# Kernel tuning notes

Measured on AMD Instinct MI355X. Metric: run time of the kernel, lower is better.

## Reference

```python
import jax, jax.numpy as jnp
import numpy as np

B, C, P = 16, 512, 4096


def setup_inputs() -> dict:
    key = jax.random.key(0)
    ks = jax.random.split(key, 7)
    s = 1.0 / np.sqrt(C)  # torch Conv1d default init scale
    return {
        "x": jax.random.normal(ks[0], (B, C, P), dtype=jnp.float32),
        "Wq": jax.random.uniform(ks[1], (C, C), jnp.float32, -s, s),
        "bq": jax.random.uniform(ks[2], (C,), jnp.float32, -s, s),
        "Wk": jax.random.uniform(ks[3], (C, C), jnp.float32, -s, s),
        "bk": jax.random.uniform(ks[4], (C,), jnp.float32, -s, s),
        "Wv": jax.random.uniform(ks[5], (C, C), jnp.float32, -s, s),
        "bv": jax.random.uniform(ks[6], (C,), jnp.float32, -s, s),
    }


def reference(x, Wq, bq, Wk, bk, Wv, bv):
    # 1x1 Conv1d == channel-mixing GEMM: out[b,o,p] = sum_i W[o,i] x[b,i,p] + b[o]
    q = jnp.einsum('oi,bip->bop', Wq, x) + bq[None, :, None]   # [B,C,P]
    k = jnp.einsum('oi,bip->bop', Wk, x) + bk[None, :, None]   # [B,C,P]
    v = jnp.einsum('oi,bip->bop', Wv, x) + bv[None, :, None]   # [B,C,P]
    energy = jnp.einsum('bcp,bdp->bcd', q, k)                  # [B,C,C] (unscaled)
    attn = jax.nn.softmax(energy, axis=-1)
    out = jnp.einsum('bcd,bdp->bcp', attn, v)                  # [B,C,P]
    return out
```

## Files before the change

kernel.cpp:

```cpp
#include <hip/hip_runtime.h>
#include <hip/hip_bf16.h>

#define CD 512
#define PD 4096
#define BD 16
#define GKS 8
#define NTRI 10

typedef __bf16 bf16x8 __attribute__((ext_vector_type(8)));
typedef float f32x4 __attribute__((ext_vector_type(4)));
typedef unsigned short u16x8 __attribute__((ext_vector_type(8)));
typedef unsigned short u16x4 __attribute__((ext_vector_type(4)));

__device__ __forceinline__ unsigned short f2bf(float f) {
  unsigned u = __builtin_bit_cast(unsigned, f);
  u += 0x7FFFu + ((u >> 16) & 1u);
  return (unsigned short)(u >> 16);
}
__device__ __forceinline__ float bf2f(unsigned short h) {
  unsigned u = ((unsigned)h) << 16;
  return __builtin_bit_cast(float, u);
}

__global__ void convert_w2(const float* __restrict__ Wq, const float* __restrict__ Wk,
                           const float* __restrict__ Wv,
                           unsigned short* __restrict__ Wqh, unsigned short* __restrict__ Wql,
                           unsigned short* __restrict__ Wkh, unsigned short* __restrict__ Wkl,
                           unsigned short* __restrict__ Wvh) {
  int i = blockIdx.x * 256 + threadIdx.x;
  if (i >= CD * CD) return;
  float q = Wq[i]; unsigned short qh = f2bf(q);
  Wqh[i] = qh; Wql[i] = f2bf(q - bf2f(qh));
  float k = Wk[i]; unsigned short kh = f2bf(k);
  Wkh[i] = kh; Wkl[i] = f2bf(k - bf2f(kh));
  Wvh[i] = f2bf(Wv[i]);
}

__global__ void convert_x(const float* __restrict__ x, unsigned short* __restrict__ xsh,
                          unsigned short* __restrict__ xsl, unsigned short* __restrict__ xth,
                          float* __restrict__ r_part) {
  __shared__ float tile[64][65];
  int z = blockIdx.z;
  int c0 = blockIdx.y * 64, p0 = blockIdx.x * 64;
  const float* xb = x + (size_t)z * CD * PD;
  int t = threadIdx.x;
  int tr = t >> 4, tc = t & 15;
  float psum[4];
#pragma unroll
  for (int j = 0; j < 4; ++j) {
    int r = tr + j * 16;
    const float* src = xb + (size_t)(c0 + r) * PD + p0 + tc * 4;
    float s = 0.f;
#pragma unroll
    for (int i = 0; i < 4; ++i) {
      float v = src[i];
      tile[r][tc * 4 + i] = v;
      s += v;
    }
    psum[j] = s;
  }
#pragma unroll
  for (int j = 0; j < 4; ++j) {
    float s = psum[j];
    s += __shfl_xor(s, 1);
    s += __shfl_xor(s, 2);
    s += __shfl_xor(s, 4);
    s += __shfl_xor(s, 8);
    if (tc == 0)
      r_part[((size_t)z * CD + c0 + tr + j * 16) * 64 + (p0 >> 6)] = s;
  }
  __syncthreads();
#pragma unroll
  for (int j = 0; j < 4; ++j) {
    int r = tr + j * 16;
    u16x4 hv, lv;
#pragma unroll
    for (int i = 0; i < 4; ++i) {
      float v = tile[r][tc * 4 + i];
      unsigned short h = f2bf(v);
      hv[i] = h; lv[i] = f2bf(v - bf2f(h));
    }
    size_t o = (size_t)z * CD * PD + (size_t)(c0 + r) * PD + p0 + tc * 4;
    *reinterpret_cast<u16x4*>(xsh + o) = hv;
    *reinterpret_cast<u16x4*>(xsl + o) = lv;
  }
#pragma unroll
  for (int j = 0; j < 4; ++j) {
    int pr = tr + j * 16;
    u16x4 hv;
#pragma unroll
    for (int i = 0; i < 4; ++i) hv[i] = f2bf(tile[tc * 4 + i][pr]);
    size_t o = (size_t)z * PD * CD + (size_t)(p0 + pr) * CD + c0 + tc * 4;
    *reinterpret_cast<u16x4*>(xth + o) = hv;
  }
}

__global__ void uvw_kernel(const float* __restrict__ r_part, const float* __restrict__ Wq,
                           const float* __restrict__ bq, const float* __restrict__ Wk,
                           float* __restrict__ uw) {
  __shared__ float rl[CD];
  int z = blockIdx.x, rg = blockIdx.y;
  int t = threadIdx.x;
  for (int c = t; c < CD; c += 256) {
    const float* rp = r_part + ((size_t)z * CD + c) * 64;
    f32x4 s4 = *reinterpret_cast<const f32x4*>(rp);
#pragma unroll
    for (int pb = 4; pb < 64; pb += 4) s4 += *reinterpret_cast<const f32x4*>(rp + pb);
    rl[c] = s4[0] + s4[1] + s4[2] + s4[3];
  }
  __syncthreads();
  int lane = t & 63, w = t >> 6;
#pragma unroll
  for (int rr = 0; rr < 16; ++rr) {
    int c = rg * 64 + w * 16 + rr;
    const float* wq = Wq + (size_t)c * CD;
    const float* wk = Wk + (size_t)c * CD;
    float du = 0.f, dw = 0.f;
#pragma unroll
    for (int j = 0; j < 8; ++j) {
      float rv = rl[lane + 64 * j];
      du += wq[lane + 64 * j] * rv;
      dw += wk[lane + 64 * j] * rv;
    }
#pragma unroll
    for (int o = 32; o > 0; o >>= 1) {
      du += __shfl_xor(du, o);
      dw += __shfl_xor(dw, o);
    }
    if (lane == 0) {
      uw[(size_t)z * 2 * CD + c] = du + (float)PD * bq[c];
      uw[(size_t)z * 2 * CD + CD + c] = dw;
    }
  }
}

enum { EPI_F32 = 0, EPI_HILO = 1, EPI_V = 2 };

template <int BM, int BN, int WM, int WN, bool SPLIT, int EPI, bool TRI, int SPLITK = 1>
__global__ __launch_bounds__((BM / WM) * (BN / WN) * 64) void gemm2(
    const unsigned short* __restrict__ Ahi, const unsigned short* __restrict__ Alo,
    const unsigned short* __restrict__ Bhi, const unsigned short* __restrict__ Blo,
    long long sA, long long sB, int ldA, int ldB, int K,
    float* __restrict__ Cf, unsigned short* __restrict__ Chi, unsigned short* __restrict__ Clo,
    long long sC, int ldC, const float* __restrict__ bias, int gx, int gy) {
  constexpr int BK = 64;
  constexpr int WAVES = (BM / WM) * (BN / WN);
  constexpr int NS = SPLIT ? 2 : 1;
  constexpr int MI = WM / 16, NI = WN / 16;
  constexpr int NWN = BN / WN;
  constexpr int CA = BM / 8, CB = BN / 8;
  constexpr int TOT = NS * (CA + CB);
  constexpr bool COMPACT = TRI && (SPLITK > 1);
  __shared__ unsigned short lds[NS * (BM + BN) * BK];

  int nwg = gridDim.x;
  int b = blockIdx.x;
  int q = nwg >> 3, r = nwg & 7, xcd = b & 7, pos = b >> 3;
  int wg = (xcd < r ? xcd * (q + 1) : r * (q + 1) + (xcd - r) * q) + pos;
  int bx, by, z, zc, tpi = 0, kbase = 0;
  if constexpr (TRI) {
    int tri = gy * (gy + 1) / 2;
    int perz = tri * SPLITK;
    z = wg / perz;
    int rem = wg - z * perz;
    int ks = rem / tri;
    tpi = rem - ks * tri;
    int tp = tpi;
    bx = 0;
    while (tp >= gy - bx) { tp -= gy - bx; ++bx; }
    by = bx + tp;
    kbase = ks * K;
    zc = z * SPLITK + ks;
  } else {
    by = wg % gy;
    int t2 = wg / gy;
    bx = t2 % gx;
    z = t2 / gx;
    zc = z;
  }

  const unsigned short* pA0 = Ahi + (size_t)z * sA + (size_t)bx * BM * ldA;
  const unsigned short* pB0 = Bhi + (size_t)z * sB + (size_t)by * BN * ldB;
  const unsigned short* pA1 = SPLIT ? Alo + (size_t)z * sA + (size_t)bx * BM * ldA : pA0;
  const unsigned short* pB1 = SPLIT ? Blo + (size_t)z * sB + (size_t)by * BN * ldB : pB0;

  int tid = threadIdx.x;
  int lane = tid & 63, wid = tid >> 6;
  int wr = wid / NWN, wc = wid % NWN;
  int lr = lane & 15, kh2 = lane >> 4;

  f32x4 acc[MI][NI] = {};

  for (int k0 = kbase; k0 < kbase + K; k0 += BK) {
#pragma unroll
    for (int i = 0; i < TOT / WAVES; ++i) {
      int c = wid + i * WAVES;
      const unsigned short* srcb; int ldX, lofs, rb2;
      if (c < CA)            { srcb = pA0; ldX = ldA; lofs = c * 512;                  rb2 = c * 8; }
      else if (c < NS * CA)  { srcb = pA1; ldX = ldA; lofs = BM * BK + (c - CA) * 512; rb2 = (c - CA) * 8; }
      else if (c < NS * CA + CB) { int cc = c - NS * CA; srcb = pB0; ldX = ldB;
                                   lofs = NS * BM * BK + cc * 512;                     rb2 = cc * 8; }
      else                   { int cc = c - NS * CA - CB; srcb = pB1; ldX = ldB;
                               lofs = NS * BM * BK + BN * BK + cc * 512;               rb2 = cc * 8; }
      int row = rb2 + (lane >> 3);
      const unsigned short* src =
          srcb + (size_t)row * ldX + k0 + (((lane & 7) ^ (row & 7)) << 3);
      __builtin_amdgcn_global_load_lds(
          (const __attribute__((address_space(1))) void*)src,
          (__attribute__((address_space(3))) void*)(lds + lofs), 16, 0, 0);
    }
    __syncthreads();

#pragma unroll
    for (int kk = 0; kk < BK / 32; ++kk) {
      bf16x8 ah[MI], al[MI], bh[NI], bl[NI];
#pragma unroll
      for (int m = 0; m < MI; ++m) {
        int row = wr * WM + m * 16 + lr;
        int so = ((((kk << 2) | kh2) ^ (row & 7)) << 3);
        ah[m] = *reinterpret_cast<const bf16x8*>(&lds[row * BK + so]);
        if constexpr (SPLIT)
          al[m] = *reinterpret_cast<const bf16x8*>(&lds[BM * BK + row * BK + so]);
      }
#pragma unroll
      for (int n = 0; n < NI; ++n) {
        int row = wc * WN + n * 16 + lr;
        int so = ((((kk << 2) | kh2) ^ (row & 7)) << 3);
        bh[n] = *reinterpret_cast<const bf16x8*>(&lds[NS * BM * BK + row * BK + so]);
        if constexpr (SPLIT)
          bl[n] = *reinterpret_cast<const bf16x8*>(&lds[NS * BM * BK + BN * BK + row * BK + so]);
      }
#pragma unroll
      for (int m = 0; m < MI; ++m)
#pragma unroll
        for (int n = 0; n < NI; ++n) {
          acc[m][n] = __builtin_amdgcn_mfma_f32_16x16x32_bf16(ah[m], bh[n], acc[m][n], 0, 0, 0);
          if constexpr (SPLIT) {
            acc[m][n] = __builtin_amdgcn_mfma_f32_16x16x32_bf16(ah[m], bl[n], acc[m][n], 0, 0, 0);
            acc[m][n] = __builtin_amdgcn_mfma_f32_16x16x32_bf16(al[m], bh[n], acc[m][n], 0, 0, 0);
          }
        }
    }
    __syncthreads();
  }

  int lg = lane >> 4;
#pragma unroll
  for (int m = 0; m < MI; ++m)
#pragma unroll
    for (int n = 0; n < NI; ++n) {
      int lcol = wc * WN + n * 16 + lr;
      float bcol = (EPI == EPI_V) ? bias[by * BN + lcol] : 0.f;
#pragma unroll
      for (int r4 = 0; r4 < 4; ++r4) {
        int lrow = wr * WM + m * 16 + lg * 4 + r4;
        float v = acc[m][n][r4];
        if constexpr (COMPACT) {
          size_t idx = (size_t)zc * sC + (size_t)tpi * (BM * BN) + (size_t)lrow * BN + lcol;
          Cf[idx] = v;
        } else {
          size_t idx = (size_t)zc * sC + (size_t)(bx * BM + lrow) * ldC + (by * BN + lcol);
          if constexpr (EPI == EPI_F32) {
            Cf[idx] = v;
          } else if constexpr (EPI == EPI_HILO) {
            unsigned short h = f2bf(v);
            Chi[idx] = h;
            Clo[idx] = f2bf(v - bf2f(h));
          } else {
            Chi[idx] = f2bf(v + bcol);
          }
        }
      }
    }
}

template <int KS>
__global__ void gram_reduce(const float* __restrict__ Gp,
                            unsigned short* __restrict__ Ghi, unsigned short* __restrict__ Glo) {
  int z = blockIdx.y;
  int tp = blockIdx.x;
  int b2 = tp, bx = 0;
  while (b2 >= 4 - bx) { b2 -= 4 - bx; ++bx; }
  int by = bx + b2;
  int t = threadIdx.x;
  const float* base = Gp + ((size_t)z * KS * NTRI + tp) * (128 * 128);
  size_t gb = (size_t)z * CD * CD;
#pragma unroll
  for (int it = 0; it < 16; ++it) {
    int lrow = it * 8 + (t >> 5);
    int lc = (t & 31) * 4;
    f32x4 s = *reinterpret_cast<const f32x4*>(base + (size_t)lrow * 128 + lc);
#pragma unroll
    for (int ks = 1; ks < KS; ++ks)
      s += *reinterpret_cast<const f32x4*>(base + (size_t)ks * NTRI * 128 * 128 +
                                           (size_t)lrow * 128 + lc);
    u16x4 h, l;
#pragma unroll
    for (int i = 0; i < 4; ++i) {
      unsigned short hh = f2bf(s[i]);
      h[i] = hh; l[i] = f2bf(s[i] - bf2f(hh));
    }
    size_t o = gb + (size_t)(bx * 128 + lrow) * CD + by * 128 + lc;
    *reinterpret_cast<u16x4*>(Ghi + o) = h;
    *reinterpret_cast<u16x4*>(Glo + o) = l;
  }
}

__global__ void mirror_g(unsigned short* __restrict__ Ghi, unsigned short* __restrict__ Glo) {
  __shared__ unsigned short shh[64][72], shl[64][72];
  int z = blockIdx.y;
  int pidx = blockIdx.x >> 2, sub = blockIdx.x & 3;
  int bx = 0, tp = pidx;
  while (tp >= 3 - bx) { tp -= 3 - bx; ++bx; }
  int by = bx + 1 + tp;
  int ti = bx * 2 + (sub & 1), tj = by * 2 + (sub >> 1);
  int t = threadIdx.x;
  int rr = t >> 2, cg = (t & 3) * 16;
  size_t gbase = (size_t)z * CD * CD;
  size_t so = gbase + (size_t)(ti * 64 + rr) * CD + tj * 64 + cg;
  *reinterpret_cast<u16x8*>(&shh[rr][cg]) = *reinterpret_cast<const u16x8*>(Ghi + so);
  *reinterpret_cast<u16x8*>(&shh[rr][cg + 8]) = *reinterpret_cast<const u16x8*>(Ghi + so + 8);
  *reinterpret_cast<u16x8*>(&shl[rr][cg]) = *reinterpret_cast<const u16x8*>(Glo + so);
  *reinterpret_cast<u16x8*>(&shl[rr][cg + 8]) = *reinterpret_cast<const u16x8*>(Glo + so + 8);
  __syncthreads();
  u16x8 oh, ol;
  size_t dst = gbase + (size_t)(tj * 64 + rr) * CD + ti * 64 + cg;
#pragma unroll
  for (int half = 0; half < 2; ++half) {
#pragma unroll
    for (int i = 0; i < 8; ++i) {
      oh[i] = shh[cg + half * 8 + i][rr];
      ol[i] = shl[cg + half * 8 + i][rr];
    }
    *reinterpret_cast<u16x8*>(Ghi + dst + half * 8) = oh;
    *reinterpret_cast<u16x8*>(Glo + dst + half * 8) = ol;
  }
}

__global__ void softmax_rows(const float* __restrict__ E, unsigned short* __restrict__ attn,
                             const float* __restrict__ bq, const float* __restrict__ bk,
                             const float* __restrict__ uw) {
  int lane = threadIdx.x & 63, wid = threadIdx.x >> 6;
  size_t row = (size_t)blockIdx.x * 4 + wid;
  int z = (int)(row >> 9), c = (int)(row & 511);
  float uc = uw[(size_t)z * 2 * CD + c];
  float bqc = bq[c];
  const float* wp = uw + (size_t)z * 2 * CD + CD;
  const float* e = E + row * CD;
  int d0 = lane * 8;
  const float4* ep = reinterpret_cast<const float4*>(e + d0);
  float4 a = ep[0], b4 = ep[1];
  float4 k0 = *reinterpret_cast<const float4*>(bk + d0);
  float4 k1 = *reinterpret_cast<const float4*>(bk + d0 + 4);
  float4 w0 = *reinterpret_cast<const float4*>(wp + d0);
  float4 w1 = *reinterpret_cast<const float4*>(wp + d0 + 4);
  float v[8] = {a.x + uc * k0.x + bqc * w0.x, a.y + uc * k0.y + bqc * w0.y,
                a.z + uc * k0.z + bqc * w0.z, a.w + uc * k0.w + bqc * w0.w,
                b4.x + uc * k1.x + bqc * w1.x, b4.y + uc * k1.y + bqc * w1.y,
                b4.z + uc * k1.z + bqc * w1.z, b4.w + uc * k1.w + bqc * w1.w};
  float m = v[0];
#pragma unroll
  for (int i = 1; i < 8; ++i) m = fmaxf(m, v[i]);
  for (int o = 32; o > 0; o >>= 1) m = fmaxf(m, __shfl_xor(m, o));
  float s = 0.f;
#pragma unroll
  for (int i = 0; i < 8; ++i) { v[i] = __expf(v[i] - m); s += v[i]; }
  for (int o = 32; o > 0; o >>= 1) s += __shfl_xor(s, o);
  float rinv = 1.0f / s;
  u16x4 h0, h1;
#pragma unroll
  for (int i = 0; i < 4; ++i) { h0[i] = f2bf(v[i] * rinv); h1[i] = f2bf(v[4 + i] * rinv); }
  unsigned short* op = attn + row * CD + d0;
  *reinterpret_cast<u16x4*>(op) = h0;
  *reinterpret_cast<u16x4*>(op + 4) = h1;
}

extern "C" void kernel_launch(void* const* d_in, const int* in_sizes, int n_in,
                              void* d_out, int out_size, void* d_ws, size_t ws_size,
                              hipStream_t stream) {
  (void)in_sizes; (void)n_in; (void)out_size;
  const float* x  = (const float*)d_in[0];
  const float* Wq = (const float*)d_in[1];
  const float* bq = (const float*)d_in[2];
  const float* Wk = (const float*)d_in[3];
  const float* bk = (const float*)d_in[4];
  const float* Wv = (const float*)d_in[5];
  const float* bv = (const float*)d_in[6];
  float* out = (float*)d_out;

  char* base = (char*)d_ws;
  size_t off = 0;
  auto carve = [&](size_t bytes) -> char* {
    char* p = base + off;
    off += (bytes + 255) & ~(size_t)255;
    return p;
  };
  const size_t WB = (size_t)CD * CD * 2;
  unsigned short* Wqh = (unsigned short*)carve(WB);
  unsigned short* Wql = (unsigned short*)carve(WB);
  unsigned short* Wkh = (unsigned short*)carve(WB);
  unsigned short* Wkl = (unsigned short*)carve(WB);
  unsigned short* Wvh = (unsigned short*)carve(WB);

  const size_t CP = (size_t)CD * PD;
  const size_t GG = (size_t)CD * CD;
  const size_t EE = (size_t)CD * CD;
  const size_t per_batch = 3 * CP * 2 + 4 * GG * 2 + (size_t)CD * 64 * 4 + 2 * CD * 4 +
                           EE * 4 + EE * 2 + CP * 2 + 4096;
  size_t rem = (ws_size > off + 4096) ? (ws_size - off - 4096) : 0;
  int nb = (int)(rem / per_batch);
  if (nb < 1) nb = 1;
  if (nb > BD) nb = BD;

  unsigned short* xsh = (unsigned short*)carve((size_t)nb * CP * 2);
  unsigned short* xsl = (unsigned short*)carve((size_t)nb * CP * 2);
  unsigned short* xth = (unsigned short*)carve((size_t)nb * CP * 2);
  unsigned short* Ghi = (unsigned short*)carve((size_t)nb * GG * 2);
  unsigned short* Glo = (unsigned short*)carve((size_t)nb * GG * 2);
  unsigned short* Thi = (unsigned short*)carve((size_t)nb * GG * 2);
  unsigned short* Tlo = (unsigned short*)carve((size_t)nb * GG * 2);
  float*          r_part = (float*)carve((size_t)nb * CD * 64 * 4);
  float*          uw  = (float*)carve((size_t)nb * 2 * CD * 4);
  float*          E   = (float*)carve((size_t)nb * EE * 4);
  unsigned short* att = (unsigned short*)carve((size_t)nb * EE * 2);
  unsigned short* vT  = (unsigned short*)carve((size_t)nb * CP * 2);

  float* Gpart = E;

  convert_w2<<<dim3((CD * CD + 255) / 256), 256, 0, stream>>>(
      Wq, Wk, Wv, Wqh, Wql, Wkh, Wkl, Wvh);

  for (int b0 = 0; b0 < BD; b0 += nb) {
    int cb = (BD - b0 < nb) ? (BD - b0) : nb;

    convert_x<<<dim3(PD / 64, CD / 64, cb), 256, 0, stream>>>(
        x + (size_t)b0 * CP, xsh, xsl, xth, r_part);

    uvw_kernel<<<dim3(cb, 8), 256, 0, stream>>>(r_part, Wq, bq, Wk, uw);

    gemm2<128, 128, 64, 32, true, EPI_F32, true, GKS><<<NTRI * GKS * cb, 512, 0, stream>>>(
        xsh, xsl, xsh, xsl, (long long)CP, (long long)CP, PD, PD, PD / GKS,
        Gpart, nullptr, nullptr, (long long)NTRI * 128 * 128, 128, nullptr, 4, 4);

    gram_reduce<GKS><<<dim3(NTRI, cb), 256, 0, stream>>>(Gpart, Ghi, Glo);

    mirror_g<<<dim3(24, cb), 256, 0, stream>>>(Ghi, Glo);

    gemm2<64, 64, 32, 32, true, EPI_HILO, false><<<8 * 8 * cb, 256, 0, stream>>>(
        Wqh, Wql, Ghi, Glo, 0, (long long)GG, CD, CD, CD,
        nullptr, Thi, Tlo, (long long)GG, CD, nullptr, 8, 8);

    gemm2<64, 64, 32, 32, true, EPI_F32, false><<<8 * 8 * cb, 256, 0, stream>>>(
        Thi, Tlo, Wkh, Wkl, (long long)GG, 0, CD, CD, CD,
        E, nullptr, nullptr, (long long)EE, CD, nullptr, 8, 8);

    softmax_rows<<<dim3(cb * CD / 4), 256, 0, stream>>>(E, att, bq, bk, uw);

    gemm2<128, 128, 64, 64, false, EPI_V, false><<<32 * 4 * cb, 256, 0, stream>>>(
        xth, nullptr, Wvh, nullptr, (long long)CP, 0, CD, CD, CD,
        nullptr, vT, nullptr, (long long)CP, CD, bv, 32, 4);

    gemm2<128, 128, 64, 64, false, EPI_F32, false><<<4 * 32 * cb, 256, 0, stream>>>(
        att, nullptr, vT, nullptr, (long long)EE, (long long)CP, CD, CD, CD,
        out + (size_t)b0 * CP, nullptr, nullptr, (long long)CP, PD, nullptr, 4, 32);
  }
}
```

Before: 354.0 us.

## Reassociate attn·(Wv·x) as (attn·Wv)·x with folded bias term

Instead of computing V = Wv·x + bv over all P (a CxCxP GEMM) and then attn·V, the code first forms attn·Wv (a small CxC GEMM) and then multiplies by x, adding a per-row bias attn·bv computed inside the softmax kernel. This removes one full C×C×P GEMM and the vT intermediate buffer. It also gives Gpart its own buffer instead of aliasing E, and vectorises convert_x loads and stores. The cost is an extra bf16 rounding of attn·Wv before the final GEMM, which may change accuracy.

```diff
diff --git a/kernel.cpp b/kernel.cpp
--- a/kernel.cpp
+++ b/kernel.cpp
@@ -23,17 +23,30 @@
 }
 
 __global__ void convert_w2(const float* __restrict__ Wq, const float* __restrict__ Wk,
-                           const float* __restrict__ Wv,
                            unsigned short* __restrict__ Wqh, unsigned short* __restrict__ Wql,
-                           unsigned short* __restrict__ Wkh, unsigned short* __restrict__ Wkl,
-                           unsigned short* __restrict__ Wvh) {
+                           unsigned short* __restrict__ Wkh, unsigned short* __restrict__ Wkl) {
   int i = blockIdx.x * 256 + threadIdx.x;
   if (i >= CD * CD) return;
   float q = Wq[i]; unsigned short qh = f2bf(q);
   Wqh[i] = qh; Wql[i] = f2bf(q - bf2f(qh));
   float k = Wk[i]; unsigned short kh = f2bf(k);
   Wkh[i] = kh; Wkl[i] = f2bf(k - bf2f(kh));
-  Wvh[i] = f2bf(Wv[i]);
+}
+
+__global__ void transpose_wv(const float* __restrict__ Wv, unsigned short* __restrict__ Wvt) {
+  __shared__ float tile[64][65];
+  int o0 = blockIdx.x * 64, j0 = blockIdx.y * 64;
+  int t = threadIdx.x, r = t >> 2, g = t & 3;
+  const float* src = Wv + (size_t)(o0 + r) * CD + j0 + g * 16;
+#pragma unroll
+  for (int i = 0; i < 16; ++i) tile[r][g * 16 + i] = src[i];
+  __syncthreads();
+  u16x8 th[2];
+#pragma unroll
+  for (int i = 0; i < 16; ++i) th[i >> 3][i & 7] = f2bf(tile[g * 16 + i][r]);
+  unsigned short* dst = Wvt + (size_t)(j0 + r) * CD + o0 + g * 16;
+  *reinterpret_cast<u16x8*>(dst) = th[0];
+  *reinterpret_cast<u16x8*>(dst + 8) = th[1];
 }
 
 __global__ void convert_x(const float* __restrict__ x, unsigned short* __restrict__ xsh,
@@ -42,57 +55,45 @@
   __shared__ float tile[64][65];
   int z = blockIdx.z;
   int c0 = blockIdx.y * 64, p0 = blockIdx.x * 64;
-  const float* xb = x + (size_t)z * CD * PD;
-  int t = threadIdx.x;
-  int tr = t >> 4, tc = t & 15;
-  float psum[4];
+  int t = threadIdx.x, r = t >> 2, g = t & 3;
+  const float* src = x + (size_t)z * CD * PD + (size_t)(c0 + r) * PD + p0 + g * 16;
+  f32x4 v4[4];
+  float s = 0.f;
 #pragma unroll
   for (int j = 0; j < 4; ++j) {
-    int r = tr + j * 16;
-    const float* src = xb + (size_t)(c0 + r) * PD + p0 + tc * 4;
-    float s = 0.f;
+    v4[j] = *reinterpret_cast<const f32x4*>(src + j * 4);
 #pragma unroll
     for (int i = 0; i < 4; ++i) {
-      float v = src[i];
-      tile[r][tc * 4 + i] = v;
-      s += v;
-    }
-    psum[j] = s;
-  }
-#pragma unroll
-  for (int j = 0; j < 4; ++j) {
-    float s = psum[j];
-    s += __shfl_xor(s, 1);
-    s += __shfl_xor(s, 2);
-    s += __shfl_xor(s, 4);
-    s += __shfl_xor(s, 8);
-    if (tc == 0)
-      r_part[((size_t)z * CD + c0 + tr + j * 16) * 64 + (p0 >> 6)] = s;
-  }
+      tile[r][g * 16 + j * 4 + i] = v4[j][i];
+      s += v4[j][i];
+    }
+  }
+  s += __shfl_xor(s, 1);
+  s += __shfl_xor(s, 2);
+  if (g == 0) r_part[((size_t)z * CD + c0 + r) * 64 + (p0 >> 6)] = s;
+  u16x8 h[2], l[2];
+#pragma unroll
+  for (int j = 0; j < 4; ++j)
+#pragma unroll
+    for (int i = 0; i < 4; ++i) {
+      int e = j * 4 + i;
+      float f = v4[j][i];
+      unsigned short hh = f2bf(f);
+      h[e >> 3][e & 7] = hh;
+      l[e >> 3][e & 7] = f2bf(f - bf2f(hh));
+    }
+  size_t so = (size_t)z * CD * PD + (size_t)(c0 + r) * PD + p0 + g * 16;
+  *reinterpret_cast<u16x8*>(xsh + so) = h[0];
+  *reinterpret_cast<u16x8*>(xsh + so + 8) = h[1];
+  *reinterpret_cast<u16x8*>(xsl + so) = l[0];
+  *reinterpret_cast<u16x8*>(xsl + so + 8) = l[1];
   __syncthreads();
-#pragma unroll
-  for (int j = 0; j < 4; ++j) {
-    int r = tr + j * 16;
-    u16x4 hv, lv;
-#pragma unroll
-    for (int i = 0; i < 4; ++i) {
-      float v = tile[r][tc * 4 + i];
-      unsigned short h = f2bf(v);
-      hv[i] = h; lv[i] = f2bf(v - bf2f(h));
-    }
-    size_t o = (size_t)z * CD * PD + (size_t)(c0 + r) * PD + p0 + tc * 4;
-    *reinterpret_cast<u16x4*>(xsh + o) = hv;
-    *reinterpret_cast<u16x4*>(xsl + o) = lv;
-  }
-#pragma unroll
-  for (int j = 0; j < 4; ++j) {
-    int pr = tr + j * 16;
-    u16x4 hv;
-#pragma unroll
-    for (int i = 0; i < 4; ++i) hv[i] = f2bf(tile[tc * 4 + i][pr]);
-    size_t o = (size_t)z * PD * CD + (size_t)(p0 + pr) * CD + c0 + tc * 4;
-    *reinterpret_cast<u16x4*>(xth + o) = hv;
-  }
+  u16x8 th[2];
+#pragma unroll
+  for (int i = 0; i < 16; ++i) th[i >> 3][i & 7] = f2bf(tile[g * 16 + i][r]);
+  size_t to = (size_t)z * PD * CD + (size_t)(p0 + r) * CD + c0 + g * 16;
+  *reinterpret_cast<u16x8*>(xth + to) = th[0];
+  *reinterpret_cast<u16x8*>(xth + to + 8) = th[1];
 }
 
 __global__ void uvw_kernel(const float* __restrict__ r_part, const float* __restrict__ Wq,
@@ -134,7 +135,7 @@
   }
 }
 
-enum { EPI_F32 = 0, EPI_HILO = 1, EPI_V = 2 };
+enum { EPI_F32 = 0, EPI_HILO = 1, EPI_BF16 = 2, EPI_ROWB = 3 };
 
 template <int BM, int BN, int WM, int WN, bool SPLIT, int EPI, bool TRI, int SPLITK = 1>
 __global__ __launch_bounds__((BM / WM) * (BN / WN) * 64) void gemm2(
@@ -250,7 +251,6 @@
 #pragma unroll
     for (int n = 0; n < NI; ++n) {
       int lcol = wc * WN + n * 16 + lr;
-      float bcol = (EPI == EPI_V) ? bias[by * BN + lcol] : 0.f;
 #pragma unroll
       for (int r4 = 0; r4 < 4; ++r4) {
         int lrow = wr * WM + m * 16 + lg * 4 + r4;
@@ -262,12 +262,14 @@
           size_t idx = (size_t)zc * sC + (size_t)(bx * BM + lrow) * ldC + (by * BN + lcol);
           if constexpr (EPI == EPI_F32) {
             Cf[idx] = v;
+          } else if constexpr (EPI == EPI_ROWB) {
+            Cf[idx] = v + bias[(size_t)zc * CD + bx * BM + lrow];
           } else if constexpr (EPI == EPI_HILO) {
             unsigned short h = f2bf(v);
             Chi[idx] = h;
             Clo[idx] = f2bf(v - bf2f(h));
           } else {
-            Chi[idx] = f2bf(v + bcol);
+            Chi[idx] = f2bf(v);
           }
         }
       }
@@ -339,7 +341,8 @@
 
 __global__ void softmax_rows(const float* __restrict__ E, unsigned short* __restrict__ attn,
                              const float* __restrict__ bq, const float* __restrict__ bk,
-                             const float* __restrict__ uw) {
+                             const float* __restrict__ uw, const float* __restrict__ bv,
+                             float* __restrict__ sv) {
   int lane = threadIdx.x & 63, wid = threadIdx.x >> 6;
   size_t row = (size_t)blockIdx.x * 4 + wid;
   int z = (int)(row >> 9), c = (int)(row & 511);
@@ -367,9 +370,18 @@
   for (int i = 0; i < 8; ++i) { v[i] = __expf(v[i] - m); s += v[i]; }
   for (int o = 32; o > 0; o >>= 1) s += __shfl_xor(s, o);
   float rinv = 1.0f / s;
+  float4 bv0 = *reinterpret_cast<const float4*>(bv + d0);
+  float4 bv1 = *reinterpret_cast<const float4*>(bv + d0 + 4);
   u16x4 h0, h1;
-#pragma unroll
-  for (int i = 0; i < 4; ++i) { h0[i] = f2bf(v[i] * rinv); h1[i] = f2bf(v[4 + i] * rinv); }
+  float svp = 0.f;
+#pragma unroll
+  for (int i = 0; i < 4; ++i) {
+    h0[i] = f2bf(v[i] * rinv);
+    h1[i] = f2bf(v[4 + i] * rinv);
+    svp += bf2f(h0[i]) * (&bv0.x)[i] + bf2f(h1[i]) * (&bv1.x)[i];
+  }
+  for (int o = 32; o > 0; o >>= 1) svp += __shfl_xor(svp, o);
+  if (lane == 0) sv[row] = svp;
   unsigned short* op = attn + row * CD + d0;
   *reinterpret_cast<u16x4*>(op) = h0;
   *reinterpret_cast<u16x4*>(op + 4) = h1;
@@ -400,13 +412,15 @@
   unsigned short* Wql = (unsigned short*)carve(WB);
   unsigned short* Wkh = (unsigned short*)carve(WB);
   unsigned short* Wkl = (unsigned short*)carve(WB);
-  unsigned short* Wvh = (unsigned short*)carve(WB);
+  unsigned short* Wvt = (unsigned short*)carve(WB);
 
   const size_t CP = (size_t)CD * PD;
   const size_t GG = (size_t)CD * CD;
   const size_t EE = (size_t)CD * CD;
+  const size_t PERZC = (size_t)NTRI * 128 * 128;
+  const size_t GPB = (size_t)GKS * PERZC;
   const size_t per_batch = 3 * CP * 2 + 4 * GG * 2 + (size_t)CD * 64 * 4 + 2 * CD * 4 +
-                           EE * 4 + EE * 2 + CP * 2 + 4096;
+                           (size_t)CD * 4 + EE * 4 + EE * 2 + GPB * 4 + 8192;
   size_t rem = (ws_size > off + 4096) ? (ws_size - off - 4096) : 0;
   int nb = (int)(rem / per_batch);
   if (nb < 1) nb = 1;
@@ -421,14 +435,13 @@
   unsigned short* Tlo = (unsigned short*)carve((size_t)nb * GG * 2);
   float*          r_part = (float*)carve((size_t)nb * CD * 64 * 4);
   float*          uw  = (float*)carve((size_t)nb * 2 * CD * 4);
+  float*          sv  = (float*)carve((size_t)nb * CD * 4);
   float*          E   = (float*)carve((size_t)nb * EE * 4);
   unsigned short* att = (unsigned short*)carve((size_t)nb * EE * 2);
-  unsigned short* vT  = (unsigned short*)carve((size_t)nb * CP * 2);
-
-  float* Gpart = E;
-
-  convert_w2<<<dim3((CD * CD + 255) / 256), 256, 0, stream>>>(
-      Wq, Wk, Wv, Wqh, Wql, Wkh, Wkl, Wvh);
+  float*          Gpart = (float*)carve((size_t)nb * GPB * 4);
+
+  convert_w2<<<dim3((CD * CD + 255) / 256), 256, 0, stream>>>(Wq, Wk, Wqh, Wql, Wkh, Wkl);
+  transpose_wv<<<dim3(8, 8), 256, 0, stream>>>(Wv, Wvt);
 
   for (int b0 = 0; b0 < BD; b0 += nb) {
     int cb = (BD - b0 < nb) ? (BD - b0) : nb;
@@ -440,7 +453,7 @@
 
     gemm2<128, 128, 64, 32, true, EPI_F32, true, GKS><<<NTRI * GKS * cb, 512, 0, stream>>>(
         xsh, xsl, xsh, xsl, (long long)CP, (long long)CP, PD, PD, PD / GKS,
-        Gpart, nullptr, nullptr, (long long)NTRI * 128 * 128, 128, nullptr, 4, 4);
+        Gpart, nullptr, nullptr, (long long)PERZC, 128, nullptr, 4, 4);
 
     gram_reduce<GKS><<<dim3(NTRI, cb), 256, 0, stream>>>(Gpart, Ghi, Glo);
 
@@ -454,14 +467,14 @@
         Thi, Tlo, Wkh, Wkl, (long long)GG, 0, CD, CD, CD,
         E, nullptr, nullptr, (long long)EE, CD, nullptr, 8, 8);
 
-    softmax_rows<<<dim3(cb * CD / 4), 256, 0, stream>>>(E, att, bq, bk, uw);
-
-    gemm2<128, 128, 64, 64, false, EPI_V, false><<<32 * 4 * cb, 256, 0, stream>>>(
-        xth, nullptr, Wvh, nullptr, (long long)CP, 0, CD, CD, CD,
-        nullptr, vT, nullptr, (long long)CP, CD, bv, 32, 4);
-
-    gemm2<128, 128, 64, 64, false, EPI_F32, false><<<4 * 32 * cb, 256, 0, stream>>>(
-        att, nullptr, vT, nullptr, (long long)EE, (long long)CP, CD, CD, CD,
-        out + (size_t)b0 * CP, nullptr, nullptr, (long long)CP, PD, nullptr, 4, 32);
-  }
-}
+    softmax_rows<<<dim3(cb * CD / 4), 256, 0, stream>>>(E, att, bq, bk, uw, bv, sv);
+
+    gemm2<64, 64, 32, 32, false, EPI_BF16, false><<<8 * 8 * cb, 256, 0, stream>>>(
+        att, nullptr, Wvt, nullptr, (long long)EE, 0, CD, CD, CD,
+        nullptr, Thi, nullptr, (long long)GG, CD, nullptr, 8, 8);
+
+    gemm2<128, 128, 64, 64, false, EPI_ROWB, false><<<4 * 32 * cb, 256, 0, stream>>>(
+        Thi, nullptr, xth, nullptr, (long long)GG, (long long)CP, CD, CD, CD,
+        out + (size_t)b0 * CP, nullptr, nullptr, (long long)CP, PD, sv, 4, 32);
+  }
+}
```

Result: faster. 329.7 us (-6.9%).
